# Performance work log

Hardware: AMD Instinct MI355X
Metric: run time of the kernel (lower is better)

The kernel has to match this reference:

```python
import jax, jax.numpy as jnp
import numpy as np

N = 100000      # nodes per graph batch
E = 1600000     # edges
G = 64          # graphs in batch
IN_CH = 128
HID = 128
OUT = 64
ACTS = [True, True, False, True, True, True]  # tanh after conv1,2,4,5,6; none after conv3


def setup_inputs() -> dict:
    key = jax.random.key(0)
    ks = jax.random.split(key, 16)
    inp = {
        "x1": jax.random.normal(ks[0], (N, IN_CH), jnp.float32),
        "edge_index1": jax.random.randint(ks[1], (2, E), 0, N, jnp.int32),
        "edge_attr1": jax.random.uniform(ks[2], (E,), jnp.float32),
        "batch1": jnp.sort(jax.random.randint(ks[3], (N,), 0, G, jnp.int32)),
        "x2": jax.random.normal(ks[4], (N, IN_CH), jnp.float32),
        "edge_index2": jax.random.randint(ks[5], (2, E), 0, N, jnp.int32),
        "edge_attr2": jax.random.uniform(ks[6], (E,), jnp.float32),
        "batch2": jnp.sort(jax.random.randint(ks[7], (N,), 0, G, jnp.int32)),
        # shared siamese parameters
        "convW": jax.random.normal(ks[8], (6, HID, HID), jnp.float32) * 0.05,
        "convB": jnp.zeros((6, HID), jnp.float32),
        "fcW1": jax.random.normal(ks[9], (HID, OUT), jnp.float32) * 0.05,
        "fcb1": jnp.zeros((OUT,), jnp.float32),
        "fcW": jax.random.normal(ks[10], (5, OUT, OUT), jnp.float32) * 0.05,
        "fcb": jnp.zeros((5, OUT), jnp.float32),
    }
    return inp


def _tower(x, edge_index, ew, batch, convW, convB, fcW1, fcb1, fcW, fcb):
    src, dst = edge_index[0], edge_index[1]
    # add self-loops with weight 1 (GCNConv default), compute symmetric norm once
    loop = jnp.arange(N, dtype=src.dtype)
    si = jnp.concatenate([src, loop])
    di = jnp.concatenate([dst, loop])
    wa = jnp.concatenate([ew, jnp.ones((N,), ew.dtype)])
    deg = jax.ops.segment_sum(wa, di, num_segments=N)           # weighted in-degree
    dinv = jnp.where(deg > 0, jax.lax.rsqrt(deg), 0.0)
    norm = dinv[si] * wa * dinv[di]                             # [E+N]
    for i, act in enumerate(ACTS):
        xw = x @ convW[i]                                       # [N, HID]
        x = jax.ops.segment_sum(norm[:, None] * xw[si], di, num_segments=N) + convB[i]
        if act:
            x = jnp.tanh(x)
    # global mean pool over graphs
    s = jax.ops.segment_sum(x, batch, num_segments=G)
    cnt = jax.ops.segment_sum(jnp.ones((N,), x.dtype), batch, num_segments=G)
    h = s / jnp.maximum(cnt, 1.0)[:, None]                      # [G, HID]
    h = jax.nn.relu(h @ fcW1 + fcb1)
    for i in range(5):
        h = jax.nn.relu(h @ fcW[i] + fcb[i])
    return h                                                    # [G, OUT]


def reference(x1, edge_index1, edge_attr1, batch1,
              x2, edge_index2, edge_attr2, batch2,
              convW, convB, fcW1, fcb1, fcW, fcb):
    h1 = _tower(x1, edge_index1, edge_attr1, batch1, convW, convB, fcW1, fcb1, fcW, fcb)
    h2 = _tower(x2, edge_index2, edge_attr2, batch2, convW, convB, fcW1, fcb1, fcW, fcb)
    return jnp.sqrt(jnp.sum((h1 - h2) ** 2, axis=-1))           # L2 norm per graph pair
```

## Files before the change

kernel.cpp:

```cpp
#include <hip/hip_runtime.h>
#include <math.h>

constexpr int NN  = 100000;
constexpr int NE  = 1600000;
constexpr int NG  = 64;
constexpr int HID = 128;
constexpr int OUT = 64;
constexpr int SCAN_B = 256;
constexpr int NBLK = (NN + SCAN_B - 1) / SCAN_B;
static const bool hActs[6] = {true, true, false, true, true, true};

typedef __attribute__((ext_vector_type(8))) short short8;
typedef __attribute__((ext_vector_type(4))) float f32x4;

__device__ __forceinline__ unsigned short f32_to_bf16_rne(float f) {
    unsigned int u = __float_as_uint(f);
    unsigned int r = (u + 0x7fffu + ((u >> 16) & 1u)) >> 16;
    return (unsigned short)r;
}
__device__ __forceinline__ float bf16_to_f32(unsigned short h) {
    return __uint_as_float(((unsigned int)h) << 16);
}

__global__ void k_deg_init(float* deg) {
    int i = blockIdx.x * 256 + threadIdx.x;
    if (i < NN) deg[i] = 1.0f;
}

__global__ void k_deg_acc(const int* __restrict__ dst, const float* __restrict__ ew,
                          float* deg) {
    int e = blockIdx.x * 256 + threadIdx.x;
    if (e < NE) atomicAdd(&deg[dst[e]], ew[e]);
}

__global__ void k_dinv(float* deg) {
    int i = blockIdx.x * 256 + threadIdx.x;
    if (i < NN) {
        float d = deg[i];
        deg[i] = (d > 0.f) ? (1.0f / sqrtf(d)) : 0.0f;
    }
}

__global__ void k_wprep(const float* __restrict__ convW,
                        unsigned short* __restrict__ Whi,
                        unsigned short* __restrict__ Wlo) {
    int t = blockIdx.x * 256 + threadIdx.x;
    if (t >= 6 * 16384) return;
    int j    = t & 7;
    int lane = (t >> 3) & 63;
    int ct   = (t >> 9) & 7;
    int kc   = (t >> 12) & 3;
    int l    = t >> 14;
    int k = kc * 32 + (lane >> 4) * 8 + j;
    int c = ct * 16 + (lane & 15);
    float w = convW[((size_t)l * HID + k) * HID + c];
    unsigned short h = f32_to_bf16_rne(w);
    Whi[t] = h;
    Wlo[t] = f32_to_bf16_rne(w - bf16_to_f32(h));
}

__global__ void k_zero_int(int* __restrict__ p, int n) {
    int i = blockIdx.x * 256 + threadIdx.x;
    if (i < n) p[i] = 0;
}

__global__ void k_count(const int* __restrict__ dst, int* __restrict__ cnt) {
    int e = blockIdx.x * 256 + threadIdx.x;
    if (e < NE) atomicAdd(&cnt[dst[e]], 1);
}

__global__ __launch_bounds__(SCAN_B) void k_scan_block(const int* __restrict__ cnt,
                                                       int* __restrict__ rowptr,
                                                       int* __restrict__ bsum) {
    __shared__ int s[SCAN_B];
    int i = blockIdx.x * SCAN_B + threadIdx.x;
    int v = (i < NN) ? cnt[i] : 0;
    s[threadIdx.x] = v;
    __syncthreads();
    for (int off = 1; off < SCAN_B; off <<= 1) {
        int x = (threadIdx.x >= off) ? s[threadIdx.x - off] : 0;
        __syncthreads();
        s[threadIdx.x] += x;
        __syncthreads();
    }
    if (i < NN) rowptr[i + 1] = s[threadIdx.x];
    if (threadIdx.x == SCAN_B - 1) bsum[blockIdx.x] = s[threadIdx.x];
}

__global__ void k_scan_partial(int* __restrict__ bsum) {
    if (threadIdx.x == 0) {
        int acc = 0;
        for (int b = 0; b < NBLK; ++b) { int v = bsum[b]; bsum[b] = acc; acc += v; }
    }
}

__global__ void k_scan_add(const int* __restrict__ bsum, int* __restrict__ rowptr) {
    int i = blockIdx.x * SCAN_B + threadIdx.x;
    if (i < NN) rowptr[i + 1] += bsum[blockIdx.x];
    if (i == 0) rowptr[0] = 0;
}

__global__ void k_cursor(const int* __restrict__ rowptr, int* __restrict__ cursor) {
    int i = blockIdx.x * 256 + threadIdx.x;
    if (i < NN) cursor[i] = rowptr[i];
}

__global__ void k_csr_fill(const int* __restrict__ src, const int* __restrict__ dst,
                           const float* __restrict__ ew, const float* __restrict__ dinv,
                           int* __restrict__ cursor, int* __restrict__ csr_src,
                           float* __restrict__ csr_w) {
    int e = blockIdx.x * 256 + threadIdx.x;
    if (e >= NE) return;
    int s = src[e], d = dst[e];
    float w = dinv[s] * ew[e] * dinv[d];
    int pos = atomicAdd(&cursor[d], 1);
    csr_src[pos] = s;
    csr_w[pos] = w;
}

__global__ void k_bounds(const int* __restrict__ batch, int* __restrict__ start) {
    int g = threadIdx.x;
    if (g > NG) return;
    int lo = 0, hi = NN;
    while (lo < hi) {
        int mid = (lo + hi) >> 1;
        if (batch[mid] < g) lo = mid + 1; else hi = mid;
    }
    start[g] = lo;
}

__global__ __launch_bounds__(256) void k_matmul_mfma(const float* __restrict__ x,
                                                     const unsigned short* __restrict__ Whi,
                                                     const unsigned short* __restrict__ Wlo,
                                                     float* __restrict__ xw) {
    const int wid  = threadIdx.x >> 6;
    const int lane = threadIdx.x & 63;
    const long rbase = ((long)blockIdx.x * 4 + wid) * 16;
    if (rbase >= NN) return;
    const int arow = lane & 15;
    const int agrp = lane >> 4;

    f32x4 acc[8];
#pragma unroll
    for (int ct = 0; ct < 8; ++ct) acc[ct] = (f32x4){0.f, 0.f, 0.f, 0.f};

    const float* xr = x + (size_t)(rbase + arow) * HID;
#pragma unroll
    for (int kc = 0; kc < 4; ++kc) {
        float4 v0 = *(const float4*)(xr + kc * 32 + agrp * 8);
        float4 v1 = *(const float4*)(xr + kc * 32 + agrp * 8 + 4);
        float vv[8] = {v0.x, v0.y, v0.z, v0.w, v1.x, v1.y, v1.z, v1.w};
        short8 ahi, alo;
#pragma unroll
        for (int j = 0; j < 8; ++j) {
            unsigned short h = f32_to_bf16_rne(vv[j]);
            ahi[j] = (short)h;
            alo[j] = (short)f32_to_bf16_rne(vv[j] - bf16_to_f32(h));
        }
#pragma unroll
        for (int ct = 0; ct < 8; ++ct) {
            short8 bhi = *(const short8*)(Whi + (((size_t)(kc * 8 + ct)) * 64 + lane) * 8);
            short8 blo = *(const short8*)(Wlo + (((size_t)(kc * 8 + ct)) * 64 + lane) * 8);
            acc[ct] = __builtin_amdgcn_mfma_f32_16x16x32_bf16(ahi, bhi, acc[ct], 0, 0, 0);
            acc[ct] = __builtin_amdgcn_mfma_f32_16x16x32_bf16(alo, bhi, acc[ct], 0, 0, 0);
            acc[ct] = __builtin_amdgcn_mfma_f32_16x16x32_bf16(ahi, blo, acc[ct], 0, 0, 0);
        }
    }
#pragma unroll
    for (int ct = 0; ct < 8; ++ct) {
#pragma unroll
        for (int r = 0; r < 4; ++r) {
            xw[(size_t)(rbase + agrp * 4 + r) * HID + ct * 16 + (lane & 15)] = acc[ct][r];
        }
    }
}

__global__ __launch_bounds__(256) void k_gather(const float* __restrict__ xw,
                                                const int* __restrict__ rowptr,
                                                const int* __restrict__ csr_src,
                                                const float* __restrict__ csr_w,
                                                const float* __restrict__ dinv,
                                                const float* __restrict__ B,
                                                float* __restrict__ xc, int act) {
    int t = blockIdx.x * 256 + threadIdx.x;
    int n = t >> 5;
    if (n >= NN) return;
    int q = t & 31;
    const float4* xw4 = (const float4*)xw;
    float d = dinv[n];
    float nself = d * d;
    float4 sv = xw4[(size_t)n * 32 + q];
    double a0 = (double)nself * (double)sv.x;
    double a1 = (double)nself * (double)sv.y;
    double a2 = (double)nself * (double)sv.z;
    double a3 = (double)nself * (double)sv.w;
    int e1 = rowptr[n + 1];
    for (int e = rowptr[n]; e < e1; ++e) {
        int s = csr_src[e];
        double w = (double)csr_w[e];
        float4 v = xw4[(size_t)s * 32 + q];
        a0 += w * (double)v.x;
        a1 += w * (double)v.y;
        a2 += w * (double)v.z;
        a3 += w * (double)v.w;
    }
    float4 b4 = ((const float4*)B)[q];
    float4 o;
    o.x = (float)a0 + b4.x;
    o.y = (float)a1 + b4.y;
    o.z = (float)a2 + b4.z;
    o.w = (float)a3 + b4.w;
    if (act) {
        o.x = tanhf(o.x); o.y = tanhf(o.y); o.z = tanhf(o.z); o.w = tanhf(o.w);
    }
    ((float4*)xc)[(size_t)n * 32 + q] = o;
}

__global__ void k_pool(const float* __restrict__ x, const int* __restrict__ start,
                       float* __restrict__ h) {
    int g = blockIdx.x;
    int c = threadIdx.x;
    int s = start[g], e = start[g + 1];
    float acc = 0.f;
#pragma unroll 4
    for (int n = s; n < e; ++n) acc += x[(size_t)n * HID + c];
    float cnt = (float)(e - s);
    h[g * HID + c] = acc / fmaxf(cnt, 1.0f);
}

__global__ __launch_bounds__(256) void k_fc(const float* __restrict__ hpool,
                                            const float* __restrict__ fcW1,
                                            const float* __restrict__ fcb1,
                                            const float* __restrict__ fcW,
                                            const float* __restrict__ fcb,
                                            float* __restrict__ hout) {
    __shared__ float ha[NG * HID];
    __shared__ float hb[NG * OUT];
    for (int i = threadIdx.x; i < NG * HID; i += 256) ha[i] = hpool[i];
    __syncthreads();
    for (int idx = threadIdx.x; idx < NG * OUT; idx += 256) {
        int g = idx >> 6, o = idx & 63;
        float acc = fcb1[o];
        for (int k = 0; k < HID; ++k) acc += ha[g * HID + k] * fcW1[k * OUT + o];
        hb[idx] = fmaxf(acc, 0.f);
    }
    __syncthreads();
    for (int l = 0; l < 5; ++l) {
        const float* in = (l & 1) ? ha : hb;
        float* outb     = (l & 1) ? hb : ha;
        const float* W = fcW + l * OUT * OUT;
        const float* b = fcb + l * OUT;
        for (int idx = threadIdx.x; idx < NG * OUT; idx += 256) {
            int g = idx >> 6, o = idx & 63;
            float acc = b[o];
            for (int k = 0; k < OUT; ++k) acc += in[g * OUT + k] * W[k * OUT + o];
            outb[idx] = fmaxf(acc, 0.f);
        }
        __syncthreads();
    }
    for (int idx = threadIdx.x; idx < NG * OUT; idx += 256) hout[idx] = ha[idx];
}

__global__ void k_dist(const float* __restrict__ h1, const float* __restrict__ h2,
                       float* __restrict__ out) {
    int g = threadIdx.x;
    if (g >= NG) return;
    float acc = 0.f;
    for (int c = 0; c < OUT; ++c) {
        float d = h1[g * OUT + c] - h2[g * OUT + c];
        acc += d * d;
    }
    out[g] = sqrtf(acc);
}

static void run_tower(const float* x_in, const int* ei, const float* ea, const int* batch,
                      const unsigned short* Whi, const unsigned short* Wlo,
                      const float* convB,
                      const float* fcW1, const float* fcb1,
                      const float* fcW, const float* fcb,
                      float* deg, int* rowptr, int* cursor, int* cnt, int* bsum,
                      int* csr_src, float* csr_w, float* xw, float* xc,
                      float* hpool, int* start, float* hout, hipStream_t stream) {
    const int* src = ei;
    const int* dst = ei + NE;
    const int gE = (NE + 255) / 256;
    const int gN = (NN + 255) / 256;
    k_deg_init<<<gN, 256, 0, stream>>>(deg);
    k_deg_acc<<<gE, 256, 0, stream>>>(dst, ea, deg);
    k_dinv<<<gN, 256, 0, stream>>>(deg);
    k_zero_int<<<gN, 256, 0, stream>>>(cnt, NN);
    k_count<<<gE, 256, 0, stream>>>(dst, cnt);
    k_scan_block<<<NBLK, SCAN_B, 0, stream>>>(cnt, rowptr, bsum);
    k_scan_partial<<<1, 64, 0, stream>>>(bsum);
    k_scan_add<<<NBLK, SCAN_B, 0, stream>>>(bsum, rowptr);
    k_cursor<<<gN, 256, 0, stream>>>(rowptr, cursor);
    k_csr_fill<<<gE, 256, 0, stream>>>(src, dst, ea, deg, cursor, csr_src, csr_w);
    k_bounds<<<1, NG + 1, 0, stream>>>(batch, start);

    const int gMM = (NN / 16 + 3) / 4;
    const float* xin = x_in;
    for (int l = 0; l < 6; ++l) {
        k_matmul_mfma<<<gMM, 256, 0, stream>>>(xin, Whi + l * 16384, Wlo + l * 16384, xw);
        k_gather<<<(NN * 32 + 255) / 256, 256, 0, stream>>>(xw, rowptr, csr_src, csr_w,
                                                            deg, convB + l * HID, xc,
                                                            hActs[l] ? 1 : 0);
        xin = xc;
    }
    k_pool<<<NG, HID, 0, stream>>>(xc, start, hpool);
    k_fc<<<1, 256, 0, stream>>>(hpool, fcW1, fcb1, fcW, fcb, hout);
}

extern "C" void kernel_launch(void* const* d_in, const int* in_sizes, int n_in,
                              void* d_out, int out_size, void* d_ws, size_t ws_size,
                              hipStream_t stream) {
    const float* x1  = (const float*)d_in[0];
    const int*   ei1 = (const int*)d_in[1];
    const float* ea1 = (const float*)d_in[2];
    const int*   b1  = (const int*)d_in[3];
    const float* x2  = (const float*)d_in[4];
    const int*   ei2 = (const int*)d_in[5];
    const float* ea2 = (const float*)d_in[6];
    const int*   b2  = (const int*)d_in[7];
    const float* convW = (const float*)d_in[8];
    const float* convB = (const float*)d_in[9];
    const float* fcW1  = (const float*)d_in[10];
    const float* fcb1  = (const float*)d_in[11];
    const float* fcW   = (const float*)d_in[12];
    const float* fcb   = (const float*)d_in[13];
    float* out = (float*)d_out;

    float* f      = (float*)d_ws;
    float* deg    = f;
    float* csr_w  = deg + NN;
    float* xw     = csr_w + NE;
    float* xc     = xw + (size_t)NN * HID;
    float* hpool  = xc + (size_t)NN * HID;
    float* h1     = hpool + NG * HID;
    float* h2     = h1 + NG * OUT;
    int*   rowptr = (int*)(h2 + NG * OUT);
    int*   cursor = rowptr + NN + 1;
    int*   cnt    = cursor + NN;
    int*   bsum   = cnt + NN;
    int*   csr_src= bsum + NBLK;
    int*   start  = csr_src + NE;
    unsigned short* Whi = (unsigned short*)(start + NG + 1);
    unsigned short* Wlo = Whi + 6 * 16384;

    k_wprep<<<(6 * 16384 + 255) / 256, 256, 0, stream>>>(convW, Whi, Wlo);

    run_tower(x1, ei1, ea1, b1, Whi, Wlo, convB, fcW1, fcb1, fcW, fcb,
              deg, rowptr, cursor, cnt, bsum, csr_src, csr_w, xw, xc,
              hpool, start, h1, stream);
    run_tower(x2, ei2, ea2, b2, Whi, Wlo, convB, fcW1, fcb1, fcW, fcb,
              deg, rowptr, cursor, cnt, bsum, csr_src, csr_w, xw, xc,
              hpool, start, h2, stream);
    k_dist<<<1, NG, 0, stream>>>(h1, h2, out);
}
```

Measured before the change: 2.977 ms.

## Store XW intermediate in bf16 and split mean pooling across blocks with atomics

The matmul now writes its output as bf16 instead of fp32, and the gather kernel reads 8-byte bf16 vectors instead of 16-byte float4. This halves the bytes moved in the random-access neighbor gather, which is the main memory cost of each layer. Pooling is also split into 8 parts per graph that combine with atomics, and the mean division moves into the FC kernel. The cost is lower precision in the aggregated features and nondeterministic float summation order in pooling.

```diff
diff --git a/kernel.cpp b/kernel.cpp
--- a/kernel.cpp
+++ b/kernel.cpp
@@ -12,6 +12,7 @@
 
 typedef __attribute__((ext_vector_type(8))) short short8;
 typedef __attribute__((ext_vector_type(4))) float f32x4;
+typedef __attribute__((ext_vector_type(4))) unsigned short us4;
 
 __device__ __forceinline__ unsigned short f32_to_bf16_rne(float f) {
     unsigned int u = __float_as_uint(f);
@@ -132,7 +133,7 @@
 __global__ __launch_bounds__(256) void k_matmul_mfma(const float* __restrict__ x,
                                                      const unsigned short* __restrict__ Whi,
                                                      const unsigned short* __restrict__ Wlo,
-                                                     float* __restrict__ xw) {
+                                                     unsigned short* __restrict__ xwb) {
     const int wid  = threadIdx.x >> 6;
     const int lane = threadIdx.x & 63;
     const long rbase = ((long)blockIdx.x * 4 + wid) * 16;
@@ -170,12 +171,13 @@
     for (int ct = 0; ct < 8; ++ct) {
 #pragma unroll
         for (int r = 0; r < 4; ++r) {
-            xw[(size_t)(rbase + agrp * 4 + r) * HID + ct * 16 + (lane & 15)] = acc[ct][r];
+            xwb[(size_t)(rbase + agrp * 4 + r) * HID + ct * 16 + (lane & 15)] =
+                f32_to_bf16_rne(acc[ct][r]);
         }
     }
 }
 
-__global__ __launch_bounds__(256) void k_gather(const float* __restrict__ xw,
+__global__ __launch_bounds__(256) void k_gather(const unsigned short* __restrict__ xwb,
                                                 const int* __restrict__ rowptr,
                                                 const int* __restrict__ csr_src,
                                                 const float* __restrict__ csr_w,
@@ -186,25 +188,25 @@
     int n = t >> 5;
     if (n >= NN) return;
     int q = t & 31;
-    const float4* xw4 = (const float4*)xw;
+    const us4* xw4 = (const us4*)xwb;
     float d = dinv[n];
     float nself = d * d;
-    float4 sv = xw4[(size_t)n * 32 + q];
-    double a0 = (double)nself * (double)sv.x;
-    double a1 = (double)nself * (double)sv.y;
-    double a2 = (double)nself * (double)sv.z;
-    double a3 = (double)nself * (double)sv.w;
+    us4 sv = xw4[(size_t)n * 32 + q];
+    double a0 = (double)nself * (double)bf16_to_f32(sv[0]);
+    double a1 = (double)nself * (double)bf16_to_f32(sv[1]);
+    double a2 = (double)nself * (double)bf16_to_f32(sv[2]);
+    double a3 = (double)nself * (double)bf16_to_f32(sv[3]);
     int e1 = rowptr[n + 1];
     for (int e = rowptr[n]; e < e1; ++e) {
         int s = csr_src[e];
         double w = (double)csr_w[e];
-        float4 v = xw4[(size_t)s * 32 + q];
-        a0 += w * (double)v.x;
-        a1 += w * (double)v.y;
-        a2 += w * (double)v.z;
-        a3 += w * (double)v.w;
-    }
-    float4 b4 = ((const float4*)B)[q];
+        us4 v = xw4[(size_t)s * 32 + q];
+        a0 += w * (double)bf16_to_f32(v[0]);
+        a1 += w * (double)bf16_to_f32(v[1]);
+        a2 += w * (double)bf16_to_f32(v[2]);
+        a3 += w * (double)bf16_to_f32(v[3]);
+    }
+    const float4 b4 = ((const float4*)B)[q];
     float4 o;
     o.x = (float)a0 + b4.x;
     o.y = (float)a1 + b4.y;
@@ -216,19 +218,24 @@
     ((float4*)xc)[(size_t)n * 32 + q] = o;
 }
 
-__global__ void k_pool(const float* __restrict__ x, const int* __restrict__ start,
-                       float* __restrict__ h) {
+__global__ void k_pool_part(const float* __restrict__ x, const int* __restrict__ start,
+                            float* __restrict__ h) {
     int g = blockIdx.x;
+    int part = blockIdx.y;
     int c = threadIdx.x;
     int s = start[g], e = start[g + 1];
+    int len = e - s;
+    int chunk = (len + 7) >> 3;
+    int cs = s + part * chunk;
+    int ce = cs + chunk < e ? cs + chunk : e;
+    if (cs >= ce) return;
     float acc = 0.f;
-#pragma unroll 4
-    for (int n = s; n < e; ++n) acc += x[(size_t)n * HID + c];
-    float cnt = (float)(e - s);
-    h[g * HID + c] = acc / fmaxf(cnt, 1.0f);
+    for (int n = cs; n < ce; ++n) acc += x[(size_t)n * HID + c];
+    atomicAdd(&h[g * HID + c], acc);
 }
 
 __global__ __launch_bounds__(256) void k_fc(const float* __restrict__ hpool,
+                                            const int* __restrict__ start,
                                             const float* __restrict__ fcW1,
                                             const float* __restrict__ fcb1,
                                             const float* __restrict__ fcW,
@@ -236,7 +243,11 @@
                                             float* __restrict__ hout) {
     __shared__ float ha[NG * HID];
     __shared__ float hb[NG * OUT];
-    for (int i = threadIdx.x; i < NG * HID; i += 256) ha[i] = hpool[i];
+    for (int i = threadIdx.x; i < NG * HID; i += 256) {
+        int g = i >> 7;
+        float cnt = (float)(start[g + 1] - start[g]);
+        ha[i] = hpool[i] / fmaxf(cnt, 1.0f);
+    }
     __syncthreads();
     for (int idx = threadIdx.x; idx < NG * OUT; idx += 256) {
         int g = idx >> 6, o = idx & 63;
@@ -279,7 +290,7 @@
                       const float* fcW1, const float* fcb1,
                       const float* fcW, const float* fcb,
                       float* deg, int* rowptr, int* cursor, int* cnt, int* bsum,
-                      int* csr_src, float* csr_w, float* xw, float* xc,
+                      int* csr_src, float* csr_w, unsigned short* xwb, float* xc,
                       float* hpool, int* start, float* hout, hipStream_t stream) {
     const int* src = ei;
     const int* dst = ei + NE;
@@ -300,14 +311,15 @@
     const int gMM = (NN / 16 + 3) / 4;
     const float* xin = x_in;
     for (int l = 0; l < 6; ++l) {
-        k_matmul_mfma<<<gMM, 256, 0, stream>>>(xin, Whi + l * 16384, Wlo + l * 16384, xw);
-        k_gather<<<(NN * 32 + 255) / 256, 256, 0, stream>>>(xw, rowptr, csr_src, csr_w,
+        k_matmul_mfma<<<gMM, 256, 0, stream>>>(xin, Whi + l * 16384, Wlo + l * 16384, xwb);
+        k_gather<<<(NN * 32 + 255) / 256, 256, 0, stream>>>(xwb, rowptr, csr_src, csr_w,
                                                             deg, convB + l * HID, xc,
                                                             hActs[l] ? 1 : 0);
         xin = xc;
     }
-    k_pool<<<NG, HID, 0, stream>>>(xc, start, hpool);
-    k_fc<<<1, 256, 0, stream>>>(hpool, fcW1, fcb1, fcW, fcb, hout);
+    k_zero_int<<<(NG * HID + 255) / 256, 256, 0, stream>>>((int*)hpool, NG * HID);
+    k_pool_part<<<dim3(NG, 8), HID, 0, stream>>>(xc, start, hpool);
+    k_fc<<<1, 256, 0, stream>>>(hpool, start, fcW1, fcb1, fcW, fcb, hout);
 }
 
 extern "C" void kernel_launch(void* const* d_in, const int* in_sizes, int n_in,
@@ -332,8 +344,8 @@
     float* f      = (float*)d_ws;
     float* deg    = f;
     float* csr_w  = deg + NN;
-    float* xw     = csr_w + NE;
-    float* xc     = xw + (size_t)NN * HID;
+    float* xwf    = csr_w + NE;
+    float* xc     = xwf + (size_t)NN * HID;
     float* hpool  = xc + (size_t)NN * HID;
     float* h1     = hpool + NG * HID;
     float* h2     = h1 + NG * OUT;
@@ -345,14 +357,15 @@
     int*   start  = csr_src + NE;
     unsigned short* Whi = (unsigned short*)(start + NG + 1);
     unsigned short* Wlo = Whi + 6 * 16384;
+    unsigned short* xwb = (unsigned short*)xwf;
 
     k_wprep<<<(6 * 16384 + 255) / 256, 256, 0, stream>>>(convW, Whi, Wlo);
 
     run_tower(x1, ei1, ea1, b1, Whi, Wlo, convB, fcW1, fcb1, fcW, fcb,
-              deg, rowptr, cursor, cnt, bsum, csr_src, csr_w, xw, xc,
+              deg, rowptr, cursor, cnt, bsum, csr_src, csr_w, xwb, xc,
               hpool, start, h1, stream);
     run_tower(x2, ei2, ea2, b2, Whi, Wlo, convB, fcW1, fcb1, fcW, fcb,
-              deg, rowptr, cursor, cnt, bsum, csr_src, csr_w, xw, xc,
+              deg, rowptr, cursor, cnt, bsum, csr_src, csr_w, xwb, xc,
               hpool, start, h2, stream);
     k_dist<<<1, NG, 0, stream>>>(h1, h2, out);
 }
```

Result: faster. 2.578 ms (-13.4%).
